# Kernel tuning notes

Hardware: AMD Instinct MI355X
Metric: run time of the kernel (lower is better)

## Reference

```python
import jax, jax.numpy as jnp
import numpy as np

STRIDE = 2

def setup_inputs() -> dict:
    key = jax.random.key(0)
    k1, k2, k3, k4, k5 = jax.random.split(key, 5)
    B, Cin, H, W = 16, 64, 128, 128
    Cout, kh, kw = 64, 3, 3
    oh = ow = 63  # ceil((H - kh + 1) / STRIDE)
    inp = jax.random.normal(k1, (B, Cin, H, W), dtype=jnp.float32)
    fan_in = Cin * kh * kw
    weight = jax.random.normal(k2, (Cout, Cin, kh, kw), dtype=jnp.float32) / np.sqrt(fan_in)
    bias = jax.random.normal(k3, (Cout,), dtype=jnp.float32) * 0.01
    selh = jax.random.randint(k4, (oh, ow), 0, STRIDE, dtype=jnp.int32)
    selw = jax.random.randint(k5, (oh, ow), 0, STRIDE, dtype=jnp.int32)
    return {"input": inp, "weight": weight, "bias": bias, "selh": selh, "selw": selw}


def reference(input, weight, bias, selh, selw):
    # Stochastic downsampled conv: per output pixel (i,j), pick the patch at
    # row i*stride + selh[i,j], col j*stride + selw[i,j], then apply the conv GEMM.
    Cout, Cin, kh, kw = weight.shape
    oh, ow = selh.shape
    # top-left corner of the selected patch for each output pixel
    rng_h = selh + jnp.arange(0, oh * STRIDE, STRIDE, dtype=jnp.int32)[:, None]   # (oh, ow)
    rng_w = selw + jnp.arange(0, ow * STRIDE, STRIDE, dtype=jnp.int32)[None, :]   # (oh, ow)
    # full patch index grids: (oh, ow, kh, kw)
    ih = rng_h[:, :, None, None] + jnp.arange(kh, dtype=jnp.int32)[None, None, :, None]
    iw = rng_w[:, :, None, None] + jnp.arange(kw, dtype=jnp.int32)[None, None, None, :]
    # gather selected im2col patches only (avoids materializing the full unfold)
    patches = input[:, :, ih, iw]  # (B, Cin, oh, ow, kh, kw)
    out = jnp.einsum('bcyxhw,ochw->boyx', patches, weight) + bias[None, :, None, None]
    return out  # (B, Cout, oh, ow)
```

## Files before the change

kernel.cpp:

```cpp
#include <hip/hip_runtime.h>


#define B_    16
#define CIN   64
#define H_    128
#define W_    128
#define COUT  64
#define OH    63
#define OW    63
#define NPIX  (OH * OW)
#define KTOT  (CIN * 9)

typedef short  short8  __attribute__((ext_vector_type(8)));
typedef float  float4v __attribute__((ext_vector_type(4)));

__device__ inline short f2bf(float f) {
    union { float f; unsigned u; } x; x.f = f;
    unsigned r = x.u + 0x7fffu + ((x.u >> 16) & 1u);
    return (short)(r >> 16);
}

__global__ __launch_bounds__(256)
void transpose_nhwc_bf16(const float* __restrict__ in, short* __restrict__ nhwc) {
    __shared__ float T[64 * 65];
    const int tid = threadIdx.x;
    const int w0  = blockIdx.x * 64;
    const int h   = blockIdx.y;
    const int b   = blockIdx.z;

    {
        const int w4 = tid & 15;
        const int cl = tid >> 4;
#pragma unroll
        for (int i = 0; i < 4; ++i) {
            const int c = cl + 16 * i;
            const float4 v = *(const float4*)&in[((b * CIN + c) * H_ + h) * W_ + w0 + 4 * w4];
            T[c * 65 + 4 * w4 + 0] = v.x;
            T[c * 65 + 4 * w4 + 1] = v.y;
            T[c * 65 + 4 * w4 + 2] = v.z;
            T[c * 65 + 4 * w4 + 3] = v.w;
        }
    }
    __syncthreads();
    {
        const int cg = tid & 7;
        const int wl = tid >> 3;
#pragma unroll
        for (int i = 0; i < 2; ++i) {
            const int w = wl + 32 * i;
            short8 v;
#pragma unroll
            for (int t = 0; t < 8; ++t)
                v[t] = f2bf(T[(8 * cg + t) * 65 + w]);
            *(short8*)&nhwc[((b * H_ + h) * W_ + w0 + w) * CIN + 8 * cg] = v;
        }
    }
}

__global__ __launch_bounds__(576)
void transpose_wgt_bf16(const float* __restrict__ wgt, short* __restrict__ wgt_t) {
    const int o = blockIdx.x;
    const int t = threadIdx.x;
    const int c = t / 9;
    const int tap = t - c * 9;
    wgt_t[o * KTOT + tap * CIN + c] = f2bf(wgt[o * KTOT + c * 9 + tap]);
}

#define PIXT  16
#define BT    4
#define LDO   68

__global__ __launch_bounds__(256, 2)
void sconv2davg_mfma(const short* __restrict__ nhwc,
                     const short* __restrict__ wgt_t,
                     const float* __restrict__ bias,
                     const int* __restrict__ selh,
                     const int* __restrict__ selw,
                     float* __restrict__ out) {
    __shared__ __align__(16) short As[9 * 64 * 32];
    __shared__ __align__(16) short Ws[9 * 64 * 32];
    __shared__ int hb_s[PIXT], wb_s[PIXT];

    const int tid = threadIdx.x;
    const int p0  = blockIdx.x * PIXT;
    const int b0  = blockIdx.y * BT;

    if (tid < PIXT) {
        int p = p0 + tid;
        if (p > NPIX - 1) p = NPIX - 1;
        int y = p / OW;
        int x = p - y * OW;
        hb_s[tid] = 2 * y + selh[p];
        wb_s[tid] = 2 * x + selw[p];
    }
    __syncthreads();

    const int ln = tid & 15;
    const int hl = (tid >> 4) & 3;
    const int wv = tid >> 6;

    const int gm  = tid >> 2;
    const int seg = tid & 3;
    const int pl  = gm >> 2;
    const int bl  = gm & 3;
    const int gb  = b0 + bl;
    const int ih0 = hb_s[pl];
    const int iw0 = wb_s[pl];

    float4v acc[4];
#pragma unroll
    for (int j = 0; j < 4; ++j) acc[j] = (float4v){0.f, 0.f, 0.f, 0.f};

    for (int cc = 0; cc < 2; ++cc) {
        const int c0 = cc * 32;

#pragma unroll
        for (int tap = 0; tap < 9; ++tap) {
            const int kh = tap / 3, kw = tap - 3 * (tap / 3);
            const short8 v = *(const short8*)
                &nhwc[((gb * H_ + ih0 + kh) * W_ + iw0 + kw) * CIN + c0 + seg * 8];
            *(short8*)&As[tap * 2048 + gm * 32 + seg * 8] = v;
        }
#pragma unroll
        for (int tap = 0; tap < 9; ++tap) {
            const short8 v = *(const short8*)
                &wgt_t[gm * KTOT + tap * CIN + c0 + seg * 8];
            *(short8*)&Ws[tap * 2048 + gm * 32 + seg * 8] = v;
        }
        __syncthreads();

#pragma unroll
        for (int tap = 0; tap < 9; ++tap) {
            const short8 a = *(const short8*)
                &As[tap * 2048 + (16 * wv + ln) * 32 + hl * 8];
#pragma unroll
            for (int j = 0; j < 4; ++j) {
                const short8 b = *(const short8*)
                    &Ws[tap * 2048 + (16 * j + ln) * 32 + hl * 8];
                acc[j] = __builtin_amdgcn_mfma_f32_16x16x32_bf16(a, b, acc[j], 0, 0, 0);
            }
        }
        __syncthreads();
    }

    float* Ot = (float*)As;
#pragma unroll
    for (int j = 0; j < 4; ++j) {
        const float bv = bias[16 * j + ln];
#pragma unroll
        for (int r = 0; r < 4; ++r)
            Ot[(16 * wv + 4 * hl + r) * LDO + 16 * j + ln] = acc[j][r] + bv;
    }
    __syncthreads();
    {
        const int o  = tid & 63;
        const int b2 = tid >> 6;
        const int rowbase = ((b0 + b2) * COUT + o) * NPIX;
#pragma unroll
        for (int pp = 0; pp < PIXT; ++pp) {
            const int p = p0 + pp;
            if (p < NPIX)
                out[rowbase + p] = Ot[(pp * 4 + b2) * LDO + o];
        }
    }
}

#define FKC   72
#define FLDA  76
__global__ __launch_bounds__(256, 4)
void sconv2davg_fallback(const float* __restrict__ in,
                         const float* __restrict__ wgt,
                         const float* __restrict__ bias,
                         const int* __restrict__ selh,
                         const int* __restrict__ selw,
                         float* __restrict__ out) {
    __shared__ float As[64 * FLDA];
    __shared__ float Ws[64 * FLDA];
    __shared__ int hb_s[4], wb_s[4];
    const int tid = threadIdx.x;
    const int p0  = blockIdx.x * 4;
    if (tid < 4) {
        int p = p0 + tid;
        if (p > NPIX - 1) p = NPIX - 1;
        int y = p / OW;
        int x = p - y * OW;
        hb_s[tid] = 2 * y + selh[p];
        wb_s[tid] = 2 * x + selw[p];
    }
    __syncthreads();
    const int tn = tid & 15, tm = tid >> 4;
    float acc[4][4];
#pragma unroll
    for (int i = 0; i < 4; ++i)
#pragma unroll
        for (int j = 0; j < 4; ++j) acc[i][j] = 0.0f;
    for (int cc = 0; cc < 8; ++cc) {
        const int c0 = cc * 8;
#pragma unroll
        for (int it = 0; it < 18; ++it) {
            int idx = tid + it * 256;
            int m = idx / FKC, rem = idx - m * FKC;
            int cl = rem / 9, r = rem - cl * 9;
            int kh = r / 3, kw = r - kh * 3;
            As[m * FLDA + rem] =
                in[((((m & 15) * CIN) + (c0 + cl)) * H_ + hb_s[m >> 4] + kh) * W_ + wb_s[m >> 4] + kw];
        }
#pragma unroll
        for (int it = 0; it < 18; ++it) {
            int idx = tid + it * 256;
            int o = idx / FKC, kk = idx - o * FKC;
            Ws[o * FLDA + kk] = wgt[o * KTOT + cc * FKC + kk];
        }
        __syncthreads();
#pragma unroll 2
        for (int k0 = 0; k0 < FKC; k0 += 4) {
            float4 a[4], w[4];
#pragma unroll
            for (int i = 0; i < 4; ++i) a[i] = *(const float4*)&As[(4 * tm + i) * FLDA + k0];
#pragma unroll
            for (int j = 0; j < 4; ++j) w[j] = *(const float4*)&Ws[(tn + 16 * j) * FLDA + k0];
#pragma unroll
            for (int i = 0; i < 4; ++i)
#pragma unroll
                for (int j = 0; j < 4; ++j) {
                    acc[i][j] += a[i].x * w[j].x; acc[i][j] += a[i].y * w[j].y;
                    acc[i][j] += a[i].z * w[j].z; acc[i][j] += a[i].w * w[j].w;
                }
        }
        __syncthreads();
    }
    const int p = p0 + (tm >> 2);
    if (p < NPIX) {
#pragma unroll
        for (int i = 0; i < 4; ++i) {
            int b = (tm & 3) * 4 + i;
#pragma unroll
            for (int j = 0; j < 4; ++j)
                out[((b * COUT) + tn + 16 * j) * NPIX + p] = acc[i][j] + bias[tn + 16 * j];
        }
    }
}

extern "C" void kernel_launch(void* const* d_in, const int* in_sizes, int n_in,
                              void* d_out, int out_size, void* d_ws, size_t ws_size,
                              hipStream_t stream) {
    const float* in   = (const float*)d_in[0];
    const float* wgt  = (const float*)d_in[1];
    const float* bias = (const float*)d_in[2];
    const int*   selh = (const int*)d_in[3];
    const int*   selw = (const int*)d_in[4];
    float* out = (float*)d_out;

    const size_t nhwc_elems = (size_t)B_ * H_ * W_ * CIN;
    const size_t need = (nhwc_elems + (size_t)COUT * KTOT) * 2;

    if (ws_size >= need) {
        short* nhwc  = (short*)d_ws;
        short* wgt_t = nhwc + nhwc_elems;
        transpose_nhwc_bf16<<<dim3(W_ / 64, H_, B_), 256, 0, stream>>>(in, nhwc);
        transpose_wgt_bf16<<<COUT, 576, 0, stream>>>(wgt, wgt_t);
        const int ptiles = (NPIX + PIXT - 1) / PIXT;
        sconv2davg_mfma<<<dim3(ptiles, B_ / BT), 256, 0, stream>>>(
            nhwc, wgt_t, bias, selh, selw, out);
    } else {
        sconv2davg_fallback<<<(NPIX + 3) / 4, 256, 0, stream>>>(
            in, wgt, bias, selh, selw, out);
    }
}
```

Baseline: 142.0 us.

## Load MFMA operands directly from global memory and merge the repack kernels

```diff
diff --git a/kernel.cpp b/kernel.cpp
--- a/kernel.cpp
+++ b/kernel.cpp
@@ -21,7 +21,20 @@
 }
 
 __global__ __launch_bounds__(256)
-void transpose_nhwc_bf16(const float* __restrict__ in, short* __restrict__ nhwc) {
+void repack_bf16(const float* __restrict__ in, const float* __restrict__ wgt,
+                 short* __restrict__ nhwc, short* __restrict__ wgt_t) {
+    if (blockIdx.y == H_) {
+        const int bid = blockIdx.z * 2 + blockIdx.x;
+        for (int e = bid * 256 + (int)threadIdx.x; e < COUT * KTOT; e += 32 * 256) {
+            const int o   = e / KTOT;
+            const int rem = e - o * KTOT;
+            const int c   = rem / 9;
+            const int tap = rem - c * 9;
+            wgt_t[o * KTOT + tap * CIN + c] = f2bf(wgt[e]);
+        }
+        return;
+    }
+
     __shared__ float T[64 * 65];
     const int tid = threadIdx.x;
     const int w0  = blockIdx.x * 64;
@@ -57,93 +70,63 @@
     }
 }
 
-__global__ __launch_bounds__(576)
-void transpose_wgt_bf16(const float* __restrict__ wgt, short* __restrict__ wgt_t) {
-    const int o = blockIdx.x;
-    const int t = threadIdx.x;
-    const int c = t / 9;
-    const int tap = t - c * 9;
-    wgt_t[o * KTOT + tap * CIN + c] = f2bf(wgt[o * KTOT + c * 9 + tap]);
-}
-
 #define PIXT  16
 #define BT    4
-#define LDO   68
-
-__global__ __launch_bounds__(256, 2)
+#define LDO   65
+
+__global__ __launch_bounds__(256, 4)
 void sconv2davg_mfma(const short* __restrict__ nhwc,
                      const short* __restrict__ wgt_t,
                      const float* __restrict__ bias,
                      const int* __restrict__ selh,
                      const int* __restrict__ selw,
                      float* __restrict__ out) {
-    __shared__ __align__(16) short As[9 * 64 * 32];
-    __shared__ __align__(16) short Ws[9 * 64 * 32];
-    __shared__ int hb_s[PIXT], wb_s[PIXT];
+    __shared__ __align__(16) float Ot[64 * LDO];
 
     const int tid = threadIdx.x;
     const int p0  = blockIdx.x * PIXT;
     const int b0  = blockIdx.y * BT;
 
-    if (tid < PIXT) {
-        int p = p0 + tid;
-        if (p > NPIX - 1) p = NPIX - 1;
-        int y = p / OW;
-        int x = p - y * OW;
-        hb_s[tid] = 2 * y + selh[p];
-        wb_s[tid] = 2 * x + selw[p];
-    }
-    __syncthreads();
-
     const int ln = tid & 15;
     const int hl = (tid >> 4) & 3;
     const int wv = tid >> 6;
 
-    const int gm  = tid >> 2;
-    const int seg = tid & 3;
-    const int pl  = gm >> 2;
-    const int bl  = gm & 3;
-    const int gb  = b0 + bl;
-    const int ih0 = hb_s[pl];
-    const int iw0 = wb_s[pl];
+    const int m  = 16 * wv + ln;
+    const int pl = m >> 2;
+    const int bl = m & 3;
+    int p = p0 + pl;
+    if (p > NPIX - 1) p = NPIX - 1;
+    const int y   = p / OW;
+    const int x   = p - y * OW;
+    const int ih0 = 2 * y + selh[p];
+    const int iw0 = 2 * x + selw[p];
+
+    const short* A0 = &nhwc[(((b0 + bl) * H_ + ih0) * W_ + iw0) * CIN + hl * 8];
+    const short* A1 = A0 + W_ * CIN;
+    const short* A2 = A1 + W_ * CIN;
+    const short* Bp = &wgt_t[ln * KTOT + hl * 8];
 
     float4v acc[4];
 #pragma unroll
     for (int j = 0; j < 4; ++j) acc[j] = (float4v){0.f, 0.f, 0.f, 0.f};
 
+#pragma unroll
     for (int cc = 0; cc < 2; ++cc) {
         const int c0 = cc * 32;
-
 #pragma unroll
         for (int tap = 0; tap < 9; ++tap) {
-            const int kh = tap / 3, kw = tap - 3 * (tap / 3);
-            const short8 v = *(const short8*)
-                &nhwc[((gb * H_ + ih0 + kh) * W_ + iw0 + kw) * CIN + c0 + seg * 8];
-            *(short8*)&As[tap * 2048 + gm * 32 + seg * 8] = v;
-        }
-#pragma unroll
-        for (int tap = 0; tap < 9; ++tap) {
-            const short8 v = *(const short8*)
-                &wgt_t[gm * KTOT + tap * CIN + c0 + seg * 8];
-            *(short8*)&Ws[tap * 2048 + gm * 32 + seg * 8] = v;
-        }
-        __syncthreads();
-
-#pragma unroll
-        for (int tap = 0; tap < 9; ++tap) {
-            const short8 a = *(const short8*)
-                &As[tap * 2048 + (16 * wv + ln) * 32 + hl * 8];
+            const int kh = tap / 3;
+            const int kw = tap - 3 * kh;
+            const short* Ar = (kh == 0) ? A0 : ((kh == 1) ? A1 : A2);
+            const short8 a = *(const short8*)&Ar[kw * CIN + c0];
 #pragma unroll
             for (int j = 0; j < 4; ++j) {
-                const short8 b = *(const short8*)
-                    &Ws[tap * 2048 + (16 * j + ln) * 32 + hl * 8];
+                const short8 b = *(const short8*)&Bp[(16 * j) * KTOT + tap * CIN + c0];
                 acc[j] = __builtin_amdgcn_mfma_f32_16x16x32_bf16(a, b, acc[j], 0, 0, 0);
             }
         }
-        __syncthreads();
-    }
-
-    float* Ot = (float*)As;
+    }
+
 #pragma unroll
     for (int j = 0; j < 4; ++j) {
         const float bv = bias[16 * j + ln];
@@ -153,14 +136,17 @@
     }
     __syncthreads();
     {
-        const int o  = tid & 63;
-        const int b2 = tid >> 6;
-        const int rowbase = ((b0 + b2) * COUT + o) * NPIX;
-#pragma unroll
-        for (int pp = 0; pp < PIXT; ++pp) {
-            const int p = p0 + pp;
-            if (p < NPIX)
-                out[rowbase + p] = Ot[(pp * 4 + b2) * LDO + o];
+        const int pp = tid & 15;
+        const int rr = tid >> 4;
+        const int p2 = p0 + pp;
+        if (p2 < NPIX) {
+#pragma unroll
+            for (int k = 0; k < 16; ++k) {
+                const int rid = k * 16 + rr;
+                const int b2  = rid >> 6;
+                const int o   = rid & 63;
+                out[((b0 + b2) * COUT + o) * NPIX + p2] = Ot[(pp * 4 + b2) * LDO + o];
+            }
         }
     }
 }
@@ -257,8 +243,7 @@
     if (ws_size >= need) {
         short* nhwc  = (short*)d_ws;
         short* wgt_t = nhwc + nhwc_elems;
-        transpose_nhwc_bf16<<<dim3(W_ / 64, H_, B_), 256, 0, stream>>>(in, nhwc);
-        transpose_wgt_bf16<<<COUT, 576, 0, stream>>>(wgt, wgt_t);
+        repack_bf16<<<dim3(W_ / 64, H_ + 1, B_), 256, 0, stream>>>(in, wgt, nhwc, wgt_t);
         const int ptiles = (NPIX + PIXT - 1) / PIXT;
         sconv2davg_mfma<<<dim3(ptiles, B_ / BT), 256, 0, stream>>>(
             nhwc, wgt_t, bias, selh, selw, out);
```

Measured after the change: 147.9 us. 1.04x slower.
